# Performance work log

Hardware: AMD Instinct MI355X
Metric: run time of the kernel (lower is better)

The kernel has to match this reference:

```python
import jax, jax.numpy as jnp
import numpy as np


def _qkernel(r, i, j, k):
    # Build the real-valued block kernel of a quaternion dense layer.
    # r,i,j,k: [in/4, out/4] -> kernel [in, out] implementing the Hamilton product.
    col_r = jnp.concatenate([r, -i, -j, -k], axis=0)
    col_i = jnp.concatenate([i, r, -k, j], axis=0)
    col_j = jnp.concatenate([j, k, r, -i], axis=0)
    col_k = jnp.concatenate([k, -j, i, r], axis=0)
    return jnp.concatenate([col_r, col_i, col_j, col_k], axis=1)


def setup_inputs() -> dict:
    key = jax.random.key(0)
    ks = jax.random.split(key, 12)
    B, F, H = 32768, 1024, 256
    F4, H4 = F // 4, H // 4
    s_in = 1.0 / np.sqrt(F)
    s_h = 1.0 / np.sqrt(H)
    inp = {
        "x": jax.random.normal(ks[0], (B, F), dtype=jnp.float32),
        "wx_r": jax.random.normal(ks[1], (4, F4, H4), dtype=jnp.float32) * s_in,
        "wx_i": jax.random.normal(ks[2], (4, F4, H4), dtype=jnp.float32) * s_in,
        "wx_j": jax.random.normal(ks[3], (4, F4, H4), dtype=jnp.float32) * s_in,
        "wx_k": jax.random.normal(ks[4], (4, F4, H4), dtype=jnp.float32) * s_in,
        "bx": jnp.zeros((4, H), dtype=jnp.float32),
        "uh_r": jax.random.normal(ks[5], (4, H4, H4), dtype=jnp.float32) * s_h,
        "uh_i": jax.random.normal(ks[6], (4, H4, H4), dtype=jnp.float32) * s_h,
        "uh_j": jax.random.normal(ks[7], (4, H4, H4), dtype=jnp.float32) * s_h,
        "uh_k": jax.random.normal(ks[8], (4, H4, H4), dtype=jnp.float32) * s_h,
        "fco_w": jax.random.normal(ks[9], (H, H), dtype=jnp.float32) * s_h,
        "fco_b": jnp.zeros((H,), dtype=jnp.float32),
    }
    return inp


def reference(x, wx_r, wx_i, wx_j, wx_k, bx, uh_r, uh_i, uh_j, uh_k, fco_w, fco_b):
    # Single-step quaternion LSTM cell with zero initial hidden/cell state.
    # Gate order along leading axis: [forget, input, output, cell].
    Kx = jax.vmap(_qkernel)(wx_r, wx_i, wx_j, wx_k)   # [4, F, H]
    Ku = jax.vmap(_qkernel)(uh_r, uh_i, uh_j, uh_k)   # [4, H, H]
    H = bx.shape[1]
    h0 = jnp.zeros((x.shape[0], H), dtype=x.dtype)
    c0 = h0
    gx = jnp.einsum('bf,gfh->gbh', x, Kx) + bx[:, None, :]   # [4, B, H]
    gu = jnp.einsum('bh,ghk->gbk', h0, Ku)                    # [4, B, H]
    z = gx + gu
    ft = jax.nn.sigmoid(z[0])
    it = jax.nn.sigmoid(z[1])
    ot = jax.nn.sigmoid(z[2])
    at = z[3]
    c = it * jnp.tanh(at) + ft * c0
    h = ot * jnp.tanh(c)
    return h @ fco_w + fco_b
```

## Files before the change

### kernel.cpp

```cpp
#include <hip/hip_runtime.h>
#include <cstdint>
#include <cstddef>

#define WS_WP   0
#define WS_FCO  1572864
#define WS_BP   1703936
#define WS_HVP  1707008

typedef __attribute__((ext_vector_type(8))) __bf16 bf16x8;
typedef __attribute__((ext_vector_type(4))) float floatx4;

__device__ __forceinline__ unsigned short f2bf(float f) {
  unsigned int u = __builtin_bit_cast(unsigned int, f);
  u += 0x7fffu + ((u >> 16) & 1u);
  return (unsigned short)(u >> 16);
}

__device__ __forceinline__ float sigmf(float z) {
  return __builtin_amdgcn_rcpf(1.f + __expf(-z));
}
__device__ __forceinline__ float tanh_(float z) {
  return 1.f - 2.f * __builtin_amdgcn_rcpf(1.f + __expf(2.f * z));
}

__device__ __forceinline__ void gld16(const void* g, void* l) {
  __builtin_amdgcn_global_load_lds(
      (const __attribute__((address_space(1))) unsigned int*)g,
      (__attribute__((address_space(3))) unsigned int*)l, 16, 0, 0);
}

__global__ __launch_bounds__(256) void pack_k(
    const float* __restrict__ wr, const float* __restrict__ wi,
    const float* __restrict__ wj, const float* __restrict__ wk,
    const float* __restrict__ bx, const float* __restrict__ fw,
    unsigned short* __restrict__ Wp, unsigned short* __restrict__ Fp,
    float* __restrict__ bp) {
  int t = threadIdx.x;
  if (blockIdx.x < 384) {
    int gpp = blockIdx.x >> 7;
    int oct = blockIdx.x & 127;
    int gp = gpp + 1;
    int h = t;
    int hb = h >> 6, hr = h & 63;
    int f0 = oct << 3;
    int fb = f0 >> 8, fr0 = f0 & 255;
    const int   comp_t[4][4] = {{0,1,2,3},{1,0,3,2},{2,3,0,1},{3,2,1,0}};
    const float sign_t[4][4] = {{1.f,-1.f,-1.f,-1.f},{1.f,1.f,-1.f,1.f},
                                {1.f,1.f,1.f,-1.f},{1.f,-1.f,1.f,1.f}};
    const float* srcs[4] = {wr, wi, wj, wk};
    const float* s = srcs[comp_t[hb][fb]] + ((size_t)((gp << 8) + fr0)) * 64 + hr;
    float sg = sign_t[hb][fb];
    unsigned short v[8];
#pragma unroll
    for (int j = 0; j < 8; ++j) v[j] = f2bf(sg * s[(size_t)j * 64]);
    int c = h * 3 + gpp;
    int cb = c / 192, nl = c % 192;
    int kb = oct >> 2, q = oct & 3;
    int idx16 = (nl << 2) + (q ^ ((nl >> 1) & 3));
    uint4 val = make_uint4(
        (unsigned)v[0] | ((unsigned)v[1] << 16), (unsigned)v[2] | ((unsigned)v[3] << 16),
        (unsigned)v[4] | ((unsigned)v[5] << 16), (unsigned)v[6] | ((unsigned)v[7] << 16));
    *(uint4*)(Wp + (size_t)(cb * 32 + kb) * 6144 + idx16 * 8) = val;
    if (oct == 0) bp[c] = bx[(gp << 8) + h];
  } else {
    int oct = blockIdx.x - 384;
    int n = t;
    int k0 = oct << 3;
    unsigned short v[8];
#pragma unroll
    for (int j = 0; j < 8; ++j) v[j] = f2bf(fw[(size_t)(k0 + j) * 256 + n]);
    int nb = n >> 7, nl = n & 127, kb = oct >> 2, q = oct & 3;
    int idx16 = (nl << 2) + (q ^ ((nl >> 1) & 3));
    uint4 val = make_uint4(
        (unsigned)v[0] | ((unsigned)v[1] << 16), (unsigned)v[2] | ((unsigned)v[3] << 16),
        (unsigned)v[4] | ((unsigned)v[5] << 16), (unsigned)v[6] | ((unsigned)v[7] << 16));
    *(uint4*)(Fp + (size_t)((nb << 3) + kb) * 4096 + idx16 * 8) = val;
  }
}

__global__ __launch_bounds__(256, 2) void gemm1_k(
    const float* __restrict__ x, const unsigned short* __restrict__ Wp,
    const float* __restrict__ bp, unsigned short* __restrict__ hvp) {
  __shared__ char smem[57344];
  float* zep = (float*)smem;

  const int t = threadIdx.x;
  const int lane = t & 63, wid = t >> 6;
  const int wm = wid >> 1, wn = wid & 1;
  const int lrow = lane & 15, q = lane >> 4;
  const int rowt = blockIdx.x;
  const int cby = blockIdx.y;
  const int row0 = rowt * 128;
  const float* xbase = x + (size_t)row0 * 1024;
  const unsigned short* wpb = Wp + (size_t)cby * 32 * 6144;

  floatx4 acc[4][6];
#pragma unroll
  for (int i = 0; i < 4; ++i)
#pragma unroll
    for (int j = 0; j < 6; ++j) acc[i][j] = (floatx4){0.f, 0.f, 0.f, 0.f};

#define STAGE(buf, kt)                                                        \
  {                                                                           \
    char* base_ = smem + (buf) * 28672;                                       \
    float* sAf_ = (float*)base_;                                              \
    unsigned short* sBs_ = (unsigned short*)(base_ + 16384);                  \
    const unsigned short* bt_ = wpb + (size_t)(kt) * 6144;                    \
    const int k0_ = (kt) * 32;                                                \
    _Pragma("unroll")                                                         \
    for (int i_ = 0; i_ < 3; ++i_) {                                          \
      int s_ = t + i_ * 256;                                                  \
      gld16(bt_ + s_ * 8, sBs_ + s_ * 8);                                     \
    }                                                                         \
    _Pragma("unroll")                                                         \
    for (int i_ = 0; i_ < 4; ++i_) {                                          \
      int s_ = t + i_ * 256;                                                  \
      int m_ = s_ >> 3, j_ = s_ & 7, jj_ = j_ ^ (m_ & 7);                     \
      gld16(xbase + (size_t)m_ * 1024 + k0_ + jj_ * 4, sAf_ + s_ * 4);        \
    }                                                                         \
  }

  STAGE(0, 0)
  for (int kt = 0; kt < 32; ++kt) {
    __syncthreads();
    if (kt < 31) STAGE((kt + 1) & 1, kt + 1)
    char* base = smem + (kt & 1) * 28672;
    float* sAf = (float*)base;
    unsigned short* sBs = (unsigned short*)(base + 16384);
    bf16x8 af[4], bf[6];
#pragma unroll
    for (int mt = 0; mt < 4; ++mt) {
      int m = wm * 64 + mt * 16 + lrow;
      const float4 a0 = *(const float4*)(sAf + (m * 8 + ((2 * q) ^ (m & 7))) * 4);
      const float4 a1 = *(const float4*)(sAf + (m * 8 + ((2 * q + 1) ^ (m & 7))) * 4);
      bf16x8 v;
      v[0] = (__bf16)a0.x; v[1] = (__bf16)a0.y; v[2] = (__bf16)a0.z; v[3] = (__bf16)a0.w;
      v[4] = (__bf16)a1.x; v[5] = (__bf16)a1.y; v[6] = (__bf16)a1.z; v[7] = (__bf16)a1.w;
      af[mt] = v;
    }
#pragma unroll
    for (int nt = 0; nt < 6; ++nt) {
      int n = wn * 96 + nt * 16 + lrow;
      int off16 = (n << 2) + (q ^ ((n >> 1) & 3));
      bf[nt] = *(const bf16x8*)(const void*)(sBs + off16 * 8);
    }
#pragma unroll
    for (int mt = 0; mt < 4; ++mt)
#pragma unroll
      for (int nt = 0; nt < 6; ++nt)
        acc[mt][nt] = __builtin_amdgcn_mfma_f32_16x16x32_bf16(af[mt], bf[nt], acc[mt][nt], 0, 0, 0);
  }
#undef STAGE
  __syncthreads();

  const float* bp0 = bp + cby * 192;
  const int er = t >> 2, oc = t & 3;
#pragma unroll
  for (int pass = 0; pass < 2; ++pass) {
    if (wm == pass) {
#pragma unroll
      for (int mt = 0; mt < 4; ++mt)
#pragma unroll
        for (int nt = 0; nt < 6; ++nt)
#pragma unroll
          for (int r = 0; r < 4; ++r)
            zep[(mt * 16 + q * 4 + r) * 201 + wn * 96 + nt * 16 + lrow] = acc[mt][nt][r];
    }
    __syncthreads();
    int ml = pass * 64 + er;
#pragma unroll
    for (int half = 0; half < 2; ++half) {
      int oo = oc + half * 4;
      unsigned short v[8];
#pragma unroll
      for (int j = 0; j < 8; ++j) {
        int hl = oo * 8 + j;
        float zi = zep[er * 201 + hl * 3 + 0] + bp0[hl * 3 + 0];
        float zo = zep[er * 201 + hl * 3 + 1] + bp0[hl * 3 + 1];
        float zc = zep[er * 201 + hl * 3 + 2] + bp0[hl * 3 + 2];
        float it = sigmf(zi);
        float ot = sigmf(zo);
        float cc = it * tanh_(zc);
        v[j] = f2bf(ot * tanh_(cc));
      }
      int ktile = cby * 2 + (oo >> 2), qq = oo & 3;
      int idx16 = (ml << 2) + (qq ^ ((ml >> 1) & 3));
      uint4 val = make_uint4(
          (unsigned)v[0] | ((unsigned)v[1] << 16), (unsigned)v[2] | ((unsigned)v[3] << 16),
          (unsigned)v[4] | ((unsigned)v[5] << 16), (unsigned)v[6] | ((unsigned)v[7] << 16));
      *(uint4*)(hvp + (size_t)(rowt * 8 + ktile) * 4096 + idx16 * 8) = val;
    }
    __syncthreads();
  }
}

__global__ __launch_bounds__(256, 4) void gemm2_k(
    const unsigned short* __restrict__ hvp, const unsigned short* __restrict__ Fp,
    const float* __restrict__ fcob, float* __restrict__ out) {
  __shared__ unsigned short sB[32768];
  const int t = threadIdx.x;
  const int lane = t & 63, wid = t >> 6;
  const int wm = wid >> 1, wn = wid & 1;
  const int lrow = lane & 15, q = lane >> 4;
  const int mb = blockIdx.x, nb = blockIdx.y;

  const unsigned short* fpb = Fp + (size_t)nb * 32768;
#pragma unroll
  for (int i = 0; i < 16; ++i) gld16(fpb + (t + i * 256) * 8, sB + (t + i * 256) * 8);

  floatx4 acc[4][4];
#pragma unroll
  for (int i = 0; i < 4; ++i)
#pragma unroll
    for (int j = 0; j < 4; ++j) acc[i][j] = (floatx4){0.f, 0.f, 0.f, 0.f};
  __syncthreads();

#pragma unroll
  for (int kt = 0; kt < 8; ++kt) {
    const unsigned short* at_ = hvp + (size_t)(mb * 8 + kt) * 4096;
    bf16x8 af[4], bf[4];
#pragma unroll
    for (int mt = 0; mt < 4; ++mt) {
      int m = wm * 64 + mt * 16 + lrow;
      int o = (m << 2) + (q ^ ((m >> 1) & 3));
      af[mt] = *(const bf16x8*)(const void*)(at_ + o * 8);
    }
#pragma unroll
    for (int nt = 0; nt < 4; ++nt) {
      int n = wn * 64 + nt * 16 + lrow;
      int o = (n << 2) + (q ^ ((n >> 1) & 3));
      bf[nt] = *(const bf16x8*)(const void*)(sB + kt * 4096 + o * 8);
    }
#pragma unroll
    for (int mt = 0; mt < 4; ++mt)
#pragma unroll
      for (int nt = 0; nt < 4; ++nt)
        acc[mt][nt] = __builtin_amdgcn_mfma_f32_16x16x32_bf16(af[mt], bf[nt], acc[mt][nt], 0, 0, 0);
  }
#pragma unroll
  for (int nt = 0; nt < 4; ++nt) {
    int colg = nb * 128 + wn * 64 + nt * 16 + lrow;
    float bias = fcob[colg];
#pragma unroll
    for (int mt = 0; mt < 4; ++mt) {
      int rowg = mb * 128 + wm * 64 + mt * 16 + q * 4;
#pragma unroll
      for (int r = 0; r < 4; ++r)
        out[(size_t)(rowg + r) * 256 + colg] = acc[mt][nt][r] + bias;
    }
  }
}

extern "C" void kernel_launch(void* const* d_in, const int* in_sizes, int n_in,
                              void* d_out, int out_size, void* d_ws, size_t ws_size,
                              hipStream_t stream) {
  const float* x  = (const float*)d_in[0];
  const float* wr = (const float*)d_in[1];
  const float* wi = (const float*)d_in[2];
  const float* wj = (const float*)d_in[3];
  const float* wk = (const float*)d_in[4];
  const float* bx = (const float*)d_in[5];
  const float* fw = (const float*)d_in[10];
  const float* fb = (const float*)d_in[11];
  char* ws = (char*)d_ws;
  unsigned short* Wp  = (unsigned short*)(ws + WS_WP);
  unsigned short* Fp  = (unsigned short*)(ws + WS_FCO);
  float*          bp  = (float*)(ws + WS_BP);
  unsigned short* hvp = (unsigned short*)(ws + WS_HVP);
  float*          out = (float*)d_out;

  hipLaunchKernelGGL(pack_k,  dim3(416),    dim3(256), 0, stream, wr, wi, wj, wk, bx, fw, Wp, Fp, bp);
  hipLaunchKernelGGL(gemm1_k, dim3(256, 4), dim3(256), 0, stream, x, Wp, bp, hvp);
  hipLaunchKernelGGL(gemm2_k, dim3(256, 2), dim3(256), 0, stream, hvp, Fp, fb, out);
}
```

Before: 290.4 us.

## Stage x tile via registers as bf16 in LDS and shrink shared memory

The A operand (x) is no longer copied fp32 into LDS with global_load_lds. It is now loaded into registers, converted once to bf16 and written to a swizzled bf16 LDS layout after the MFMAs, so the inner loop reads bf16x8 directly and skips per-wave repeated conversion. This halves A's LDS footprint and cuts LDS to 40 KB. The epilogue is also split into four passes of 32 rows so the smaller zep buffer fits. The cost is more register pressure and synchronous global loads held in registers across the MFMA phase.

```diff
diff --git a/kernel.cpp b/kernel.cpp
--- a/kernel.cpp
+++ b/kernel.cpp
@@ -8,6 +8,7 @@
 #define WS_HVP  1707008
 
 typedef __attribute__((ext_vector_type(8))) __bf16 bf16x8;
+typedef __attribute__((ext_vector_type(4))) __bf16 bf16x4;
 typedef __attribute__((ext_vector_type(4))) float floatx4;
 
 __device__ __forceinline__ unsigned short f2bf(float f) {
@@ -81,7 +82,7 @@
 __global__ __launch_bounds__(256, 2) void gemm1_k(
     const float* __restrict__ x, const unsigned short* __restrict__ Wp,
     const float* __restrict__ bp, unsigned short* __restrict__ hvp) {
-  __shared__ char smem[57344];
+  __shared__ char smem[40960];
   float* zep = (float*)smem;
 
   const int t = threadIdx.x;
@@ -94,87 +95,107 @@
   const float* xbase = x + (size_t)row0 * 1024;
   const unsigned short* wpb = Wp + (size_t)cby * 32 * 6144;
 
+  const int sr = t >> 3, skq = t & 7;
+  const int sq8 = skq >> 1, shalf = skq & 1;
+
   floatx4 acc[4][6];
 #pragma unroll
   for (int i = 0; i < 4; ++i)
 #pragma unroll
     for (int j = 0; j < 6; ++j) acc[i][j] = (floatx4){0.f, 0.f, 0.f, 0.f};
 
-#define STAGE(buf, kt)                                                        \
+#define STAGE_B(buf, kt)                                                      \
   {                                                                           \
-    char* base_ = smem + (buf) * 28672;                                       \
-    float* sAf_ = (float*)base_;                                              \
-    unsigned short* sBs_ = (unsigned short*)(base_ + 16384);                  \
+    unsigned short* sBs_ = (unsigned short*)(smem + (buf) * 20480 + 8192);    \
     const unsigned short* bt_ = wpb + (size_t)(kt) * 6144;                    \
-    const int k0_ = (kt) * 32;                                                \
     _Pragma("unroll")                                                         \
     for (int i_ = 0; i_ < 3; ++i_) {                                          \
       int s_ = t + i_ * 256;                                                  \
       gld16(bt_ + s_ * 8, sBs_ + s_ * 8);                                     \
     }                                                                         \
+  }
+#define LOAD_A(ra, kt)                                                        \
+  {                                                                           \
+    const float* ab_ = xbase + (kt) * 32 + skq * 4;                           \
+    _Pragma("unroll")                                                         \
+    for (int i_ = 0; i_ < 4; ++i_)                                            \
+      ra[i_] = *(const float4*)(ab_ + (size_t)(i_ * 32 + sr) * 1024);         \
+  }
+#define WRITE_A(ra, buf)                                                      \
+  {                                                                           \
+    unsigned short* sAs_ = (unsigned short*)(smem + (buf) * 20480);           \
     _Pragma("unroll")                                                         \
     for (int i_ = 0; i_ < 4; ++i_) {                                          \
-      int s_ = t + i_ * 256;                                                  \
-      int m_ = s_ >> 3, j_ = s_ & 7, jj_ = j_ ^ (m_ & 7);                     \
-      gld16(xbase + (size_t)m_ * 1024 + k0_ + jj_ * 4, sAf_ + s_ * 4);        \
+      int m_ = i_ * 32 + sr;                                                  \
+      int slot_ = (m_ << 2) + (sq8 ^ ((m_ >> 1) & 3));                        \
+      bf16x4 v_;                                                              \
+      v_[0] = (__bf16)ra[i_].x; v_[1] = (__bf16)ra[i_].y;                     \
+      v_[2] = (__bf16)ra[i_].z; v_[3] = (__bf16)ra[i_].w;                     \
+      *(bf16x4*)(sAs_ + slot_ * 8 + shalf * 4) = v_;                          \
     }                                                                         \
   }
 
-  STAGE(0, 0)
+  {
+    float4 r0[4];
+    LOAD_A(r0, 0)
+    STAGE_B(0, 0)
+    WRITE_A(r0, 0)
+  }
+  float4 ra[4];
   for (int kt = 0; kt < 32; ++kt) {
     __syncthreads();
-    if (kt < 31) STAGE((kt + 1) & 1, kt + 1)
-    char* base = smem + (kt & 1) * 28672;
-    float* sAf = (float*)base;
-    unsigned short* sBs = (unsigned short*)(base + 16384);
+    if (kt < 31) {
+      LOAD_A(ra, kt + 1)
+      STAGE_B((kt + 1) & 1, kt + 1)
+    }
+    const unsigned short* sA = (const unsigned short*)(smem + (kt & 1) * 20480);
+    const unsigned short* sB = sA + 4096;
     bf16x8 af[4], bf[6];
 #pragma unroll
     for (int mt = 0; mt < 4; ++mt) {
       int m = wm * 64 + mt * 16 + lrow;
-      const float4 a0 = *(const float4*)(sAf + (m * 8 + ((2 * q) ^ (m & 7))) * 4);
-      const float4 a1 = *(const float4*)(sAf + (m * 8 + ((2 * q + 1) ^ (m & 7))) * 4);
-      bf16x8 v;
-      v[0] = (__bf16)a0.x; v[1] = (__bf16)a0.y; v[2] = (__bf16)a0.z; v[3] = (__bf16)a0.w;
-      v[4] = (__bf16)a1.x; v[5] = (__bf16)a1.y; v[6] = (__bf16)a1.z; v[7] = (__bf16)a1.w;
-      af[mt] = v;
+      int slot = (m << 2) + (q ^ ((m >> 1) & 3));
+      af[mt] = *(const bf16x8*)(const void*)(sA + slot * 8);
     }
 #pragma unroll
     for (int nt = 0; nt < 6; ++nt) {
       int n = wn * 96 + nt * 16 + lrow;
       int off16 = (n << 2) + (q ^ ((n >> 1) & 3));
-      bf[nt] = *(const bf16x8*)(const void*)(sBs + off16 * 8);
+      bf[nt] = *(const bf16x8*)(const void*)(sB + off16 * 8);
     }
 #pragma unroll
     for (int mt = 0; mt < 4; ++mt)
 #pragma unroll
       for (int nt = 0; nt < 6; ++nt)
         acc[mt][nt] = __builtin_amdgcn_mfma_f32_16x16x32_bf16(af[mt], bf[nt], acc[mt][nt], 0, 0, 0);
-  }
-#undef STAGE
+    if (kt < 31) WRITE_A(ra, (kt + 1) & 1)
+  }
+#undef STAGE_B
+#undef LOAD_A
+#undef WRITE_A
   __syncthreads();
 
   const float* bp0 = bp + cby * 192;
-  const int er = t >> 2, oc = t & 3;
-#pragma unroll
-  for (int pass = 0; pass < 2; ++pass) {
-    if (wm == pass) {
-#pragma unroll
-      for (int mt = 0; mt < 4; ++mt)
+  const int er = t >> 3, oc = t & 7;
+#pragma unroll
+  for (int pass = 0; pass < 4; ++pass) {
+    if (wm == (pass >> 1)) {
+      int mtb = (pass & 1) * 2;
+#pragma unroll
+      for (int mi = 0; mi < 2; ++mi)
 #pragma unroll
         for (int nt = 0; nt < 6; ++nt)
 #pragma unroll
           for (int r = 0; r < 4; ++r)
-            zep[(mt * 16 + q * 4 + r) * 201 + wn * 96 + nt * 16 + lrow] = acc[mt][nt][r];
+            zep[(mi * 16 + q * 4 + r) * 201 + wn * 96 + nt * 16 + lrow] = acc[mtb + mi][nt][r];
     }
     __syncthreads();
-    int ml = pass * 64 + er;
-#pragma unroll
-    for (int half = 0; half < 2; ++half) {
-      int oo = oc + half * 4;
+    {
+      int ml = pass * 32 + er;
       unsigned short v[8];
 #pragma unroll
       for (int j = 0; j < 8; ++j) {
-        int hl = oo * 8 + j;
+        int hl = oc * 8 + j;
         float zi = zep[er * 201 + hl * 3 + 0] + bp0[hl * 3 + 0];
         float zo = zep[er * 201 + hl * 3 + 1] + bp0[hl * 3 + 1];
         float zc = zep[er * 201 + hl * 3 + 2] + bp0[hl * 3 + 2];
@@ -183,7 +204,7 @@
         float cc = it * tanh_(zc);
         v[j] = f2bf(ot * tanh_(cc));
       }
-      int ktile = cby * 2 + (oo >> 2), qq = oo & 3;
+      int ktile = cby * 2 + (oc >> 2), qq = oc & 3;
       int idx16 = (ml << 2) + (qq ^ ((ml >> 1) & 3));
       uint4 val = make_uint4(
           (unsigned)v[0] | ((unsigned)v[1] << 16), (unsigned)v[2] | ((unsigned)v[3] << 16),
```

After: 328.0 us. +13.0%, slower.
